# Kernel optimization log

Measured on AMD Instinct MI355X. Metric: run time of the kernel, lower is better.

The kernel has to match this reference:

```python
import jax, jax.numpy as jnp
import numpy as np

N_ENSEMBLE = 50
STATE_DIM = 32
ACTION_DIM = 8
HIDDEN = 256
BATCH = 8192
OUT_DIM = STATE_DIM + 1  # next_state + reward


def setup_inputs() -> dict:
    key = jax.random.key(0)
    ks = jax.random.split(key, 8)
    s = 0.05  # small init scale to keep activations sane
    return {
        "state": jax.random.normal(ks[0], (BATCH, STATE_DIM), dtype=jnp.float32),
        "action": jax.random.normal(ks[1], (BATCH, ACTION_DIM), dtype=jnp.float32),
        "W1": jax.random.normal(ks[2], (N_ENSEMBLE, STATE_DIM + ACTION_DIM, HIDDEN), dtype=jnp.float32) * s,
        "b1": jnp.zeros((N_ENSEMBLE, HIDDEN), dtype=jnp.float32),
        "W2": jax.random.normal(ks[3], (N_ENSEMBLE, HIDDEN, HIDDEN), dtype=jnp.float32) * s,
        "b2": jnp.zeros((N_ENSEMBLE, HIDDEN), dtype=jnp.float32),
        "W3": jax.random.normal(ks[4], (N_ENSEMBLE, HIDDEN, HIDDEN), dtype=jnp.float32) * s,
        "b3": jnp.zeros((N_ENSEMBLE, HIDDEN), dtype=jnp.float32),
        "W4": jax.random.normal(ks[5], (N_ENSEMBLE, HIDDEN, OUT_DIM), dtype=jnp.float32) * s,
        "b4": jnp.zeros((N_ENSEMBLE, OUT_DIM), dtype=jnp.float32),
    }


def reference(state, action, W1, b1, W2, b2, W3, b3, W4, b4):
    # state_action: [B, S+A] shared across all ensemble members
    sa = jnp.concatenate((state, action), axis=1)
    # Batched-over-ensemble GEMMs replace the python loop over 50 MLPs.
    # h: [B, E, H]
    h = jax.nn.relu(jnp.einsum("bi,eih->beh", sa, W1) + b1)
    h = jax.nn.relu(jnp.einsum("beh,ehk->bek", h, W2) + b2)
    h = jax.nn.relu(jnp.einsum("beh,ehk->bek", h, W3) + b3)
    preds = jnp.einsum("beh,eho->beo", h, W4) + b4  # [B, E, S+1]
    return preds[..., :-1], preds[..., -1]
```

## Files before the change

kernel.cpp:

```cpp
#include <hip/hip_runtime.h>


typedef __attribute__((ext_vector_type(8))) short short8;
typedef __attribute__((ext_vector_type(4))) float floatx4;

#define NE 50
#define NB 8192
#define OUT_NS_ELEMS (NB * NE * 32)
#define OSTRIDE 48

__device__ __forceinline__ unsigned short f2bf_rne(float x) {
  unsigned u = __float_as_uint(x);
  u += 0x7fffu + ((u >> 16) & 1u);
  return (unsigned short)(u >> 16);
}
__device__ __forceinline__ float bf2f(unsigned short b) {
  return __uint_as_float(((unsigned)b) << 16);
}
__device__ __forceinline__ floatx4 mfma16(short8 a, short8 b, floatx4 c) {
  return __builtin_amdgcn_mfma_f32_16x16x32_bf16(a, b, c, 0, 0, 0);
}
__device__ __forceinline__ unsigned pack_bf2(float lo, float hi) {
  unsigned u0 = __float_as_uint(lo) + 0x8000u;
  unsigned u1 = __float_as_uint(hi) + 0x8000u;
  return __builtin_amdgcn_perm(u1, u0, 0x07060302u);
}

__device__ __forceinline__ unsigned short load_bf(const void* p, long i, bool isbf) {
  if (isbf) return ((const unsigned short*)p)[i];
  return f2bf_rne(((const float*)p)[i]);
}
__device__ __forceinline__ float load_f(const void* p, long i, bool isbf) {
  if (isbf) return bf2f(((const unsigned short*)p)[i]);
  return ((const float*)p)[i];
}

__device__ void pack_w_panel(const void* __restrict__ src, unsigned short* __restrict__ dst,
                             bool isbf, int e, int kt, int K, int N, int NT, int perE,
                             unsigned short* lds) {
  const int t = threadIdx.x;
  const int Npad = NT * 16;
  const int NP = Npad + 10;
  if (!isbf && N == Npad) {
    const int nq = Npad >> 2;
    for (int idx = t; idx < 32 * nq; idx += 256) {
      int r = idx / nq, q = idx - r * nq;
      int k = kt * 32 + r;
      unsigned short v0 = 0, v1 = 0, v2 = 0, v3 = 0;
      if (k < K) {
        const float4 f =
            *(const float4*)((const float*)src + ((long)(e * K + k) * N + q * 4));
        v0 = f2bf_rne(f.x); v1 = f2bf_rne(f.y);
        v2 = f2bf_rne(f.z); v3 = f2bf_rne(f.w);
      }
      unsigned* p = (unsigned*)(lds + r * NP + q * 4);
      p[0] = (unsigned)v0 | ((unsigned)v1 << 16);
      p[1] = (unsigned)v2 | ((unsigned)v3 << 16);
    }
  } else if (isbf && N == Npad) {
    const int no = Npad >> 3;
    for (int idx = t; idx < 32 * no; idx += 256) {
      int r = idx / no, q = idx - r * no;
      int k = kt * 32 + r;
      uint4 f = make_uint4(0u, 0u, 0u, 0u);
      if (k < K)
        f = *(const uint4*)((const unsigned short*)src + ((long)(e * K + k) * N + q * 8));
      unsigned* p = (unsigned*)(lds + r * NP + q * 8);
      p[0] = f.x; p[1] = f.y; p[2] = f.z; p[3] = f.w;
    }
  } else {
    for (int idx = t; idx < 32 * Npad; idx += 256) {
      int r = idx / Npad, c = idx - r * Npad;
      int k = kt * 32 + r;
      unsigned short v = 0;
      if (k < K && c < N) v = load_bf(src, (long)(e * K + k) * N + c, isbf);
      lds[r * NP + c] = v;
    }
  }
  __syncthreads();
  for (int u = t; u < NT * 64; u += 256) {
    int nt = u >> 6, kb = (u >> 4) & 3, ni = u & 15;
    int n = nt * 16 + ni;
    unsigned v[4];
#pragma unroll
    for (int p = 0; p < 4; ++p) {
      unsigned lo = lds[(kb * 8 + 2 * p) * NP + n];
      unsigned hi = lds[(kb * 8 + 2 * p + 1) * NP + n];
      v[p] = lo | (hi << 16);
    }
    long off = (long)e * perE + ((long)((kt * NT + nt) * 64 + kb * 16 + ni)) * 8;
    *(uint4*)(dst + off) = make_uint4(v[0], v[1], v[2], v[3]);
  }
}

__global__ void k_pack(const void* __restrict__ state, const void* __restrict__ action,
                       const void* __restrict__ W1, const void* __restrict__ W2,
                       const void* __restrict__ W3, const void* __restrict__ W4,
                       const void* __restrict__ b1, const void* __restrict__ b2,
                       const void* __restrict__ b3, const void* __restrict__ b4,
                       int isbfi,
                       unsigned short* __restrict__ saP, unsigned short* __restrict__ w1P,
                       unsigned short* __restrict__ w2P, unsigned short* __restrict__ w3P,
                       unsigned short* __restrict__ w4P, float* __restrict__ biasP) {
  __shared__ unsigned short lds[32 * 266];
  const bool isbf = (isbfi != 0);
  const int b = blockIdx.x;
  if (b < 400) {
    pack_w_panel(W2, w2P, isbf, b >> 3, b & 7, 256, 256, 16, 65536, lds);
  } else if (b < 800) {
    int bb = b - 400;
    pack_w_panel(W3, w3P, isbf, bb >> 3, bb & 7, 256, 256, 16, 65536, lds);
  } else if (b < 900) {
    int bb = b - 800;
    pack_w_panel(W1, w1P, isbf, bb >> 1, bb & 1, 40, 256, 16, 16384, lds);
  } else if (b < 1300) {
    int bb = b - 900;
    pack_w_panel(W4, w4P, isbf, bb >> 3, bb & 7, 256, 33, 3, 12288, lds);
  } else if (b < 1556) {
    int u = (b - 1300) * 256 + threadIdx.x;
    int mi = u & 15, kb = (u >> 4) & 7, mt = u >> 7;
    int row = mt * 16 + mi;
    unsigned v[4] = {0u, 0u, 0u, 0u};
    if (kb < 4) {
#pragma unroll
      for (int p = 0; p < 4; ++p) {
        unsigned lo = load_bf(state, (long)row * 32 + kb * 8 + 2 * p, isbf);
        unsigned hi = load_bf(state, (long)row * 32 + kb * 8 + 2 * p + 1, isbf);
        v[p] = lo | (hi << 16);
      }
    } else if (kb == 4) {
#pragma unroll
      for (int p = 0; p < 4; ++p) {
        unsigned lo = load_bf(action, (long)row * 8 + 2 * p, isbf);
        unsigned hi = load_bf(action, (long)row * 8 + 2 * p + 1, isbf);
        v[p] = lo | (hi << 16);
      }
    }
    *(uint4*)(saP + (long)u * 8) = make_uint4(v[0], v[1], v[2], v[3]);
  } else {
    int gid = (b - 1556) * 256 + threadIdx.x;
    if (gid < NE * 816) {
      int e = gid / 816, r = gid - e * 816;
      float v = 0.0f;
      if (r < 256)      v = load_f(b1, e * 256 + r,         isbf);
      else if (r < 512) v = load_f(b2, e * 256 + (r - 256), isbf);
      else if (r < 768) v = load_f(b3, e * 256 + (r - 512), isbf);
      else { int q = r - 768; if (q < 33) v = load_f(b4, e * 33 + q, isbf); }
      biasP[gid] = v;
    }
  }
}


__device__ __forceinline__ void store_tile16(const floatx4& a4, unsigned short* hT,
                                             int FT, int BT, int li, int g) {
  int k0 = FT * 16 + g * 4;
  unsigned d0 = pack_bf2(fmaxf(a4[0], 0.0f), fmaxf(a4[1], 0.0f));
  unsigned d1 = pack_bf2(fmaxf(a4[2], 0.0f), fmaxf(a4[3], 0.0f));
  int addr = ((k0 >> 5) * 4 + BT) * 512 + ((k0 >> 3) & 3) * 128 + li * 8 + (k0 & 7);
  *(unsigned long long*)(hT + addr) =
      (unsigned long long)d0 | ((unsigned long long)d1 << 32);
}

__device__ __forceinline__ void hidden_layer(const unsigned short* __restrict__ wp,
                                             const float* __restrict__ br,
                                             unsigned short* hT,
                                             int wf, int l, int li, int g) {
  floatx4 acc[4][4];
#pragma unroll
  for (int ot = 0; ot < 4; ++ot) {
    const float4 bq = *(const float4*)(br + wf * 64 + ot * 16 + g * 4);
    floatx4 iv = {bq.x, bq.y, bq.z, bq.w};
#pragma unroll
    for (int bt = 0; bt < 4; ++bt) acc[ot][bt] = iv;
  }
#pragma unroll
  for (int kt = 0; kt < 8; ++kt) {
    short8 a[4];
#pragma unroll
    for (int ot = 0; ot < 4; ++ot)
      a[ot] = *(const short8*)(wp + (long)((kt * 16 + wf * 4 + ot) * 64 + l) * 8);
#pragma unroll
    for (int bt = 0; bt < 4; ++bt) {
      short8 b = *(const short8*)(hT + ((kt * 4 + bt) * 64 + l) * 8);
#pragma unroll
      for (int ot = 0; ot < 4; ++ot)
        acc[ot][bt] = mfma16(a[ot], b, acc[ot][bt]);
    }
  }
  __syncthreads();
#pragma unroll
  for (int ot = 0; ot < 4; ++ot)
#pragma unroll
    for (int bt = 0; bt < 4; ++bt)
      store_tile16(acc[ot][bt], hT, wf * 4 + ot, bt, li, g);
  __syncthreads();
}

__global__ __launch_bounds__(256, 4) void k_mlp(
    const unsigned short* __restrict__ sa,
    const unsigned short* __restrict__ w1,
    const unsigned short* __restrict__ w2,
    const unsigned short* __restrict__ w3,
    const unsigned short* __restrict__ w4,
    const float* __restrict__ bias,
    int isbfi,
    float* __restrict__ rewardWS,
    void* __restrict__ outp) {
  __shared__ __attribute__((aligned(16))) unsigned short hT[16384];
  const int tid = threadIdx.x;
  const int wf = tid >> 6, l = tid & 63, li = l & 15, g = l >> 4;

  const int lid = blockIdx.y * 128 + blockIdx.x;
  const int swz = (lid & 7) * 800 + (lid >> 3);
  const int e  = swz >> 7;
  const int bb = swz & 127;

  const float* brow = bias + e * 816;
  const bool isbf = (isbfi != 0);

  {
    floatx4 acc[4][4];
#pragma unroll
    for (int ot = 0; ot < 4; ++ot) {
      const float4 bq = *(const float4*)(brow + wf * 64 + ot * 16 + g * 4);
      floatx4 iv = {bq.x, bq.y, bq.z, bq.w};
#pragma unroll
      for (int bt = 0; bt < 4; ++bt) acc[ot][bt] = iv;
    }
#pragma unroll
    for (int kt = 0; kt < 2; ++kt) {
      short8 a[4];
#pragma unroll
      for (int ot = 0; ot < 4; ++ot)
        a[ot] = *(const short8*)(w1 + (long)e * 16384 +
                                 (long)((kt * 16 + wf * 4 + ot) * 64 + l) * 8);
#pragma unroll
      for (int bt = 0; bt < 4; ++bt) {
        short8 b = *(const short8*)(sa + (long)((bb * 4 + bt) * 128 + kt * 64 + l) * 8);
#pragma unroll
        for (int ot = 0; ot < 4; ++ot)
          acc[ot][bt] = mfma16(a[ot], b, acc[ot][bt]);
      }
    }
#pragma unroll
    for (int ot = 0; ot < 4; ++ot)
#pragma unroll
      for (int bt = 0; bt < 4; ++bt)
        store_tile16(acc[ot][bt], hT, wf * 4 + ot, bt, li, g);
    __syncthreads();
  }

  hidden_layer(w2 + (long)e * 65536, brow + 256, hT, wf, l, li, g);
  hidden_layer(w3 + (long)e * 65536, brow + 512, hT, wf, l, li, g);

  const float* brow4 = brow + 768;
  floatx4 acc4[3];
#pragma unroll
  for (int ft = 0; ft < 3; ++ft) {
    const float4 bq = *(const float4*)(brow4 + ft * 16 + g * 4);
    floatx4 iv = {bq.x, bq.y, bq.z, bq.w};
    acc4[ft] = iv;
  }
#pragma unroll
  for (int kt = 0; kt < 8; ++kt) {
    short8 a[3];
#pragma unroll
    for (int ft = 0; ft < 3; ++ft)
      a[ft] = *(const short8*)(w4 + (long)e * 12288 + (long)((kt * 3 + ft) * 64 + l) * 8);
    short8 b = *(const short8*)(hT + ((kt * 4 + wf) * 64 + l) * 8);
#pragma unroll
    for (int ft = 0; ft < 3; ++ft)
      acc4[ft] = mfma16(a[ft], b, acc4[ft]);
  }

  if (g == 0) {
    rewardWS[(long)e * NB + bb * 64 + wf * 16 + li] = acc4[2][0];
  }

  __syncthreads();
#pragma unroll
  for (int ft = 0; ft < 2; ++ft) {
    int batch = wf * 16 + li;
    unsigned d0 = pack_bf2(acc4[ft][0], acc4[ft][1]);
    unsigned d1 = pack_bf2(acc4[ft][2], acc4[ft][3]);
    *(unsigned long long*)(hT + batch * OSTRIDE + ft * 16 + g * 4) =
        (unsigned long long)d0 | ((unsigned long long)d1 << 32);
  }
  __syncthreads();

  if (isbf) {
    unsigned short* o16 = (unsigned short*)outp;
    int batch = tid >> 2;
    int chunk = tid & 3;
    uint4 v = *(const uint4*)(hT + batch * OSTRIDE + chunk * 8);
    *(uint4*)(o16 + ((long)(bb * 64 + batch) * NE + e) * 32 + chunk * 8) = v;
  } else {
    float* o32 = (float*)outp;
#pragma unroll
    for (int p = 0; p < 2; ++p) {
      int idx = p * 256 + tid;
      int batch = idx >> 3;
      int chunk = idx & 7;
      const unsigned short* s = hT + batch * OSTRIDE + chunk * 4;
      *(float4*)(o32 + ((long)(bb * 64 + batch) * NE + e) * 32 + chunk * 4) =
          make_float4(bf2f(s[0]), bf2f(s[1]), bf2f(s[2]), bf2f(s[3]));
    }
  }
}

__global__ void k_reward(const float* __restrict__ rw, int isbfi,
                         void* __restrict__ outp) {
  int id = blockIdx.x * 256 + threadIdx.x;
  if (id >= NB * NE) return;
  int b = id / NE, e = id - b * NE;
  float v = rw[(long)e * NB + b];
  if (isbfi != 0) {
    unsigned u = __float_as_uint(v) + 0x8000u;
    ((unsigned short*)outp)[OUT_NS_ELEMS + id] = (unsigned short)(u >> 16);
  } else {
    ((float*)outp)[OUT_NS_ELEMS + id] = v;
  }
}

extern "C" void kernel_launch(void* const* d_in, const int* in_sizes, int n_in,
                              void* d_out, int out_size, void* d_ws, size_t ws_size,
                              hipStream_t stream) {
  const void* state  = d_in[0];
  const void* action = d_in[1];
  const void* W1 = d_in[2];
  const void* b1 = d_in[3];
  const void* W2 = d_in[4];
  const void* b2 = d_in[5];
  const void* W3 = d_in[6];
  const void* b3 = d_in[7];
  const void* W4 = d_in[8];
  const void* b4 = d_in[9];
  (void)n_in; (void)out_size; (void)ws_size;

  const int isbf = (in_sizes[4] == NE * 256 * 256 * 2) ? 1 : 0;

  char* ws = (char*)d_ws;
  unsigned short* saP    = (unsigned short*)(ws + 256);
  unsigned short* w1P    = (unsigned short*)(ws + 1048832);
  unsigned short* w2P    = (unsigned short*)(ws + 2687232);
  unsigned short* w3P    = (unsigned short*)(ws + 9240832);
  unsigned short* w4P    = (unsigned short*)(ws + 15794432);
  float* biasP           = (float*)(ws + 17023232);
  float* rewardWS        = (float*)(ws + 17186432);

  k_pack<<<1716, 256, 0, stream>>>(state, action, W1, W2, W3, W4, b1, b2, b3, b4,
                                   isbf, saP, w1P, w2P, w3P, w4P, biasP);
  k_mlp<<<dim3(128, 50), 256, 0, stream>>>(saP, w1P, w2P, w3P, w4P, biasP, isbf,
                                           rewardWS, d_out);
  k_reward<<<(NB * NE + 255) / 256, 256, 0, stream>>>(rewardWS, isbf, d_out);
}
```

Baseline: 236.3 us.

## Halve per-block batch tile to 32 rows to double grid and raise occupancy

Each block of the fused MLP kernel now handles 32 batch rows instead of 64. This halves the accumulator registers and the LDS hidden buffer, doubles the grid to 256x50 blocks, and raises the launch-bounds occupancy hint from 4 to 5. The final layer's work is redistributed across the four waves: two compute next-state tiles and two compute reward. The aim is more resident waves for latency hiding, paid for with twice as many weight reloads per batch row and more blocks overall.

```diff
diff --git a/kernel.cpp b/kernel.cpp
--- a/kernel.cpp
+++ b/kernel.cpp
@@ -157,7 +157,7 @@
   int k0 = FT * 16 + g * 4;
   unsigned d0 = pack_bf2(fmaxf(a4[0], 0.0f), fmaxf(a4[1], 0.0f));
   unsigned d1 = pack_bf2(fmaxf(a4[2], 0.0f), fmaxf(a4[3], 0.0f));
-  int addr = ((k0 >> 5) * 4 + BT) * 512 + ((k0 >> 3) & 3) * 128 + li * 8 + (k0 & 7);
+  int addr = ((k0 >> 5) * 2 + BT) * 512 + ((k0 >> 3) & 3) * 128 + li * 8 + (k0 & 7);
   *(unsigned long long*)(hT + addr) =
       (unsigned long long)d0 | ((unsigned long long)d1 << 32);
 }
@@ -166,13 +166,13 @@
                                              const float* __restrict__ br,
                                              unsigned short* hT,
                                              int wf, int l, int li, int g) {
-  floatx4 acc[4][4];
+  floatx4 acc[4][2];
 #pragma unroll
   for (int ot = 0; ot < 4; ++ot) {
     const float4 bq = *(const float4*)(br + wf * 64 + ot * 16 + g * 4);
     floatx4 iv = {bq.x, bq.y, bq.z, bq.w};
 #pragma unroll
-    for (int bt = 0; bt < 4; ++bt) acc[ot][bt] = iv;
+    for (int bt = 0; bt < 2; ++bt) acc[ot][bt] = iv;
   }
 #pragma unroll
   for (int kt = 0; kt < 8; ++kt) {
@@ -181,8 +181,8 @@
     for (int ot = 0; ot < 4; ++ot)
       a[ot] = *(const short8*)(wp + (long)((kt * 16 + wf * 4 + ot) * 64 + l) * 8);
 #pragma unroll
-    for (int bt = 0; bt < 4; ++bt) {
-      short8 b = *(const short8*)(hT + ((kt * 4 + bt) * 64 + l) * 8);
+    for (int bt = 0; bt < 2; ++bt) {
+      short8 b = *(const short8*)(hT + ((kt * 2 + bt) * 64 + l) * 8);
 #pragma unroll
       for (int ot = 0; ot < 4; ++ot)
         acc[ot][bt] = mfma16(a[ot], b, acc[ot][bt]);
@@ -192,12 +192,12 @@
 #pragma unroll
   for (int ot = 0; ot < 4; ++ot)
 #pragma unroll
-    for (int bt = 0; bt < 4; ++bt)
+    for (int bt = 0; bt < 2; ++bt)
       store_tile16(acc[ot][bt], hT, wf * 4 + ot, bt, li, g);
   __syncthreads();
 }
 
-__global__ __launch_bounds__(256, 4) void k_mlp(
+__global__ __launch_bounds__(256, 5) void k_mlp(
     const unsigned short* __restrict__ sa,
     const unsigned short* __restrict__ w1,
     const unsigned short* __restrict__ w2,
@@ -207,26 +207,26 @@
     int isbfi,
     float* __restrict__ rewardWS,
     void* __restrict__ outp) {
-  __shared__ __attribute__((aligned(16))) unsigned short hT[16384];
+  __shared__ __attribute__((aligned(16))) unsigned short hT[8192];
   const int tid = threadIdx.x;
   const int wf = tid >> 6, l = tid & 63, li = l & 15, g = l >> 4;
 
-  const int lid = blockIdx.y * 128 + blockIdx.x;
-  const int swz = (lid & 7) * 800 + (lid >> 3);
-  const int e  = swz >> 7;
-  const int bb = swz & 127;
+  const int lid = blockIdx.y * 256 + blockIdx.x;
+  const int swz = (lid & 7) * 1600 + (lid >> 3);
+  const int e  = swz >> 8;
+  const int bb = swz & 255;
 
   const float* brow = bias + e * 816;
   const bool isbf = (isbfi != 0);
 
   {
-    floatx4 acc[4][4];
+    floatx4 acc[4][2];
 #pragma unroll
     for (int ot = 0; ot < 4; ++ot) {
       const float4 bq = *(const float4*)(brow + wf * 64 + ot * 16 + g * 4);
       floatx4 iv = {bq.x, bq.y, bq.z, bq.w};
 #pragma unroll
-      for (int bt = 0; bt < 4; ++bt) acc[ot][bt] = iv;
+      for (int bt = 0; bt < 2; ++bt) acc[ot][bt] = iv;
     }
 #pragma unroll
     for (int kt = 0; kt < 2; ++kt) {
@@ -236,8 +236,8 @@
         a[ot] = *(const short8*)(w1 + (long)e * 16384 +
                                  (long)((kt * 16 + wf * 4 + ot) * 64 + l) * 8);
 #pragma unroll
-      for (int bt = 0; bt < 4; ++bt) {
-        short8 b = *(const short8*)(sa + (long)((bb * 4 + bt) * 128 + kt * 64 + l) * 8);
+      for (int bt = 0; bt < 2; ++bt) {
+        short8 b = *(const short8*)(sa + (long)((bb * 2 + bt) * 128 + kt * 64 + l) * 8);
 #pragma unroll
         for (int ot = 0; ot < 4; ++ot)
           acc[ot][bt] = mfma16(a[ot], b, acc[ot][bt]);
@@ -246,7 +246,7 @@
 #pragma unroll
     for (int ot = 0; ot < 4; ++ot)
 #pragma unroll
-      for (int bt = 0; bt < 4; ++bt)
+      for (int bt = 0; bt < 2; ++bt)
         store_tile16(acc[ot][bt], hT, wf * 4 + ot, bt, li, g);
     __syncthreads();
   }
@@ -255,57 +255,63 @@
   hidden_layer(w3 + (long)e * 65536, brow + 512, hT, wf, l, li, g);
 
   const float* brow4 = brow + 768;
-  floatx4 acc4[3];
-#pragma unroll
-  for (int ft = 0; ft < 3; ++ft) {
-    const float4 bq = *(const float4*)(brow4 + ft * 16 + g * 4);
-    floatx4 iv = {bq.x, bq.y, bq.z, bq.w};
-    acc4[ft] = iv;
+  const int bl = wf & 1;
+  const int nft = (wf < 2) ? 2 : 1;
+  const int f0 = (wf < 2) ? 0 : 2;
+  floatx4 acc4[2];
+#pragma unroll
+  for (int ft = 0; ft < 2; ++ft) {
+    if (ft < nft) {
+      const float4 bq = *(const float4*)(brow4 + (f0 + ft) * 16 + g * 4);
+      floatx4 iv = {bq.x, bq.y, bq.z, bq.w};
+      acc4[ft] = iv;
+    }
   }
 #pragma unroll
   for (int kt = 0; kt < 8; ++kt) {
-    short8 a[3];
-#pragma unroll
-    for (int ft = 0; ft < 3; ++ft)
-      a[ft] = *(const short8*)(w4 + (long)e * 12288 + (long)((kt * 3 + ft) * 64 + l) * 8);
-    short8 b = *(const short8*)(hT + ((kt * 4 + wf) * 64 + l) * 8);
-#pragma unroll
-    for (int ft = 0; ft < 3; ++ft)
-      acc4[ft] = mfma16(a[ft], b, acc4[ft]);
-  }
-
-  if (g == 0) {
-    rewardWS[(long)e * NB + bb * 64 + wf * 16 + li] = acc4[2][0];
-  }
-
-  __syncthreads();
-#pragma unroll
-  for (int ft = 0; ft < 2; ++ft) {
-    int batch = wf * 16 + li;
-    unsigned d0 = pack_bf2(acc4[ft][0], acc4[ft][1]);
-    unsigned d1 = pack_bf2(acc4[ft][2], acc4[ft][3]);
-    *(unsigned long long*)(hT + batch * OSTRIDE + ft * 16 + g * 4) =
-        (unsigned long long)d0 | ((unsigned long long)d1 << 32);
+    short8 b = *(const short8*)(hT + ((kt * 2 + bl) * 64 + l) * 8);
+#pragma unroll
+    for (int ft = 0; ft < 2; ++ft) {
+      if (ft < nft) {
+        short8 a = *(const short8*)(w4 + (long)e * 12288 +
+                                    (long)((kt * 3 + f0 + ft) * 64 + l) * 8);
+        acc4[ft] = mfma16(a, b, acc4[ft]);
+      }
+    }
+  }
+
+  if (wf >= 2 && g == 0) {
+    rewardWS[(long)e * NB + bb * 32 + bl * 16 + li] = acc4[0][0];
+  }
+
+  __syncthreads();
+  if (wf < 2) {
+#pragma unroll
+    for (int ft = 0; ft < 2; ++ft) {
+      int batch = bl * 16 + li;
+      unsigned d0 = pack_bf2(acc4[ft][0], acc4[ft][1]);
+      unsigned d1 = pack_bf2(acc4[ft][2], acc4[ft][3]);
+      *(unsigned long long*)(hT + batch * OSTRIDE + ft * 16 + g * 4) =
+          (unsigned long long)d0 | ((unsigned long long)d1 << 32);
+    }
   }
   __syncthreads();
 
   if (isbf) {
-    unsigned short* o16 = (unsigned short*)outp;
-    int batch = tid >> 2;
-    int chunk = tid & 3;
-    uint4 v = *(const uint4*)(hT + batch * OSTRIDE + chunk * 8);
-    *(uint4*)(o16 + ((long)(bb * 64 + batch) * NE + e) * 32 + chunk * 8) = v;
+    if (tid < 128) {
+      unsigned short* o16 = (unsigned short*)outp;
+      int batch = tid >> 2;
+      int chunk = tid & 3;
+      uint4 v = *(const uint4*)(hT + batch * OSTRIDE + chunk * 8);
+      *(uint4*)(o16 + ((long)(bb * 32 + batch) * NE + e) * 32 + chunk * 8) = v;
+    }
   } else {
     float* o32 = (float*)outp;
-#pragma unroll
-    for (int p = 0; p < 2; ++p) {
-      int idx = p * 256 + tid;
-      int batch = idx >> 3;
-      int chunk = idx & 7;
-      const unsigned short* s = hT + batch * OSTRIDE + chunk * 4;
-      *(float4*)(o32 + ((long)(bb * 64 + batch) * NE + e) * 32 + chunk * 4) =
-          make_float4(bf2f(s[0]), bf2f(s[1]), bf2f(s[2]), bf2f(s[3]));
-    }
+    int batch = tid >> 3;
+    int chunk = tid & 7;
+    const unsigned short* s = hT + batch * OSTRIDE + chunk * 4;
+    *(float4*)(o32 + ((long)(bb * 32 + batch) * NE + e) * 32 + chunk * 4) =
+        make_float4(bf2f(s[0]), bf2f(s[1]), bf2f(s[2]), bf2f(s[3]));
   }
 }
 
@@ -351,7 +357,7 @@
 
   k_pack<<<1716, 256, 0, stream>>>(state, action, W1, W2, W3, W4, b1, b2, b3, b4,
                                    isbf, saP, w1P, w2P, w3P, w4P, biasP);
-  k_mlp<<<dim3(128, 50), 256, 0, stream>>>(saP, w1P, w2P, w3P, w4P, biasP, isbf,
+  k_mlp<<<dim3(256, 50), 256, 0, stream>>>(saP, w1P, w2P, w3P, w4P, biasP, isbf,
                                            rewardWS, d_out);
   k_reward<<<(NB * NE + 255) / 256, 256, 0, stream>>>(rewardWS, isbf, d_out);
 }
```

Result: slower. 276.6 us (+17.1%).

## Switch hidden layers from 16x16x32 to 32x32x16 bf16 MFMA tiles

Applied to the files above, without the earlier changes.

Replaces the 16x16x32 MFMA tiling of layers 1-3 with 32x32x16 MFMA. Each wave now computes a 2x2 grid of 32x32 output tiles instead of a 4x4 grid of 16x16 tiles. The weight and input packing, the activation LDS layout and the store routine are rewritten to match the 32x32 operand fragment layout, and the layer-4 B-operand read is re-indexed accordingly. The aim is fewer MFMA issues and fewer LDS and global operand loads per FLOP. The risk is different LDS bank-conflict patterns and longer MFMA dependency latency.

```diff
diff --git a/kernel.cpp b/kernel.cpp
--- a/kernel.cpp
+++ b/kernel.cpp
@@ -3,6 +3,7 @@
 
 typedef __attribute__((ext_vector_type(8))) short short8;
 typedef __attribute__((ext_vector_type(4))) float floatx4;
+typedef __attribute__((ext_vector_type(16))) float floatx16;
 
 #define NE 50
 #define NB 8192
@@ -20,6 +21,9 @@
 __device__ __forceinline__ floatx4 mfma16(short8 a, short8 b, floatx4 c) {
   return __builtin_amdgcn_mfma_f32_16x16x32_bf16(a, b, c, 0, 0, 0);
 }
+__device__ __forceinline__ floatx16 mfma32(short8 a, short8 b, floatx16 c) {
+  return __builtin_amdgcn_mfma_f32_32x32x16_bf16(a, b, c, 0, 0, 0);
+}
 __device__ __forceinline__ unsigned pack_bf2(float lo, float hi) {
   unsigned u0 = __float_as_uint(lo) + 0x8000u;
   unsigned u1 = __float_as_uint(hi) + 0x8000u;
@@ -36,8 +40,8 @@
 }
 
 __device__ void pack_w_panel(const void* __restrict__ src, unsigned short* __restrict__ dst,
-                             bool isbf, int e, int kt, int K, int N, int NT, int perE,
-                             unsigned short* lds) {
+                             bool isbf, bool fmt32, int e, int kt, int K, int N, int NT,
+                             int perE, unsigned short* lds) {
   const int t = threadIdx.x;
   const int Npad = NT * 16;
   const int NP = Npad + 10;
@@ -78,18 +82,40 @@
     }
   }
   __syncthreads();
-  for (int u = t; u < NT * 64; u += 256) {
-    int nt = u >> 6, kb = (u >> 4) & 3, ni = u & 15;
-    int n = nt * 16 + ni;
-    unsigned v[4];
-#pragma unroll
-    for (int p = 0; p < 4; ++p) {
-      unsigned lo = lds[(kb * 8 + 2 * p) * NP + n];
-      unsigned hi = lds[(kb * 8 + 2 * p + 1) * NP + n];
-      v[p] = lo | (hi << 16);
-    }
-    long off = (long)e * perE + ((long)((kt * NT + nt) * 64 + kb * 16 + ni)) * 8;
-    *(uint4*)(dst + off) = make_uint4(v[0], v[1], v[2], v[3]);
+  if (fmt32) {
+    const int NMT = NT >> 1;
+    const int per_ku = NMT * 64;
+    for (int u = t; u < NT * 64; u += 256) {
+      int ku_loc = u / per_ku;
+      int rem = u - ku_loc * per_ku;
+      int mu = rem >> 6, lane = rem & 63;
+      int m = mu * 32 + (lane & 31);
+      int rowbase = ku_loc * 16 + (lane >> 5) * 8;
+      unsigned v[4];
+#pragma unroll
+      for (int p = 0; p < 4; ++p) {
+        unsigned lo = lds[(rowbase + 2 * p) * NP + m];
+        unsigned hi = lds[(rowbase + 2 * p + 1) * NP + m];
+        v[p] = lo | (hi << 16);
+      }
+      long off = (long)e * perE +
+                 ((long)(((kt * 2 + ku_loc) * NMT + mu) * 64 + lane)) * 8;
+      *(uint4*)(dst + off) = make_uint4(v[0], v[1], v[2], v[3]);
+    }
+  } else {
+    for (int u = t; u < NT * 64; u += 256) {
+      int nt = u >> 6, kb = (u >> 4) & 3, ni = u & 15;
+      int n = nt * 16 + ni;
+      unsigned v[4];
+#pragma unroll
+      for (int p = 0; p < 4; ++p) {
+        unsigned lo = lds[(kb * 8 + 2 * p) * NP + n];
+        unsigned hi = lds[(kb * 8 + 2 * p + 1) * NP + n];
+        v[p] = lo | (hi << 16);
+      }
+      long off = (long)e * perE + ((long)((kt * NT + nt) * 64 + kb * 16 + ni)) * 8;
+      *(uint4*)(dst + off) = make_uint4(v[0], v[1], v[2], v[3]);
+    }
   }
 }
 
@@ -106,33 +132,34 @@
   const bool isbf = (isbfi != 0);
   const int b = blockIdx.x;
   if (b < 400) {
-    pack_w_panel(W2, w2P, isbf, b >> 3, b & 7, 256, 256, 16, 65536, lds);
+    pack_w_panel(W2, w2P, isbf, true, b >> 3, b & 7, 256, 256, 16, 65536, lds);
   } else if (b < 800) {
     int bb = b - 400;
-    pack_w_panel(W3, w3P, isbf, bb >> 3, bb & 7, 256, 256, 16, 65536, lds);
+    pack_w_panel(W3, w3P, isbf, true, bb >> 3, bb & 7, 256, 256, 16, 65536, lds);
   } else if (b < 900) {
     int bb = b - 800;
-    pack_w_panel(W1, w1P, isbf, bb >> 1, bb & 1, 40, 256, 16, 16384, lds);
+    pack_w_panel(W1, w1P, isbf, true, bb >> 1, bb & 1, 40, 256, 16, 16384, lds);
   } else if (b < 1300) {
     int bb = b - 900;
-    pack_w_panel(W4, w4P, isbf, bb >> 3, bb & 7, 256, 33, 3, 12288, lds);
+    pack_w_panel(W4, w4P, isbf, false, bb >> 3, bb & 7, 256, 33, 3, 12288, lds);
   } else if (b < 1556) {
     int u = (b - 1300) * 256 + threadIdx.x;
-    int mi = u & 15, kb = (u >> 4) & 7, mt = u >> 7;
-    int row = mt * 16 + mi;
+    int lane = u & 63, ku = (u >> 6) & 3, bt32 = u >> 8;
+    int n = bt32 * 32 + (lane & 31);
+    int kb = ku * 16 + (lane >> 5) * 8;
     unsigned v[4] = {0u, 0u, 0u, 0u};
-    if (kb < 4) {
+    if (kb < 32) {
 #pragma unroll
       for (int p = 0; p < 4; ++p) {
-        unsigned lo = load_bf(state, (long)row * 32 + kb * 8 + 2 * p, isbf);
-        unsigned hi = load_bf(state, (long)row * 32 + kb * 8 + 2 * p + 1, isbf);
+        unsigned lo = load_bf(state, (long)n * 32 + kb + 2 * p, isbf);
+        unsigned hi = load_bf(state, (long)n * 32 + kb + 2 * p + 1, isbf);
         v[p] = lo | (hi << 16);
       }
-    } else if (kb == 4) {
+    } else if (kb == 32) {
 #pragma unroll
       for (int p = 0; p < 4; ++p) {
-        unsigned lo = load_bf(action, (long)row * 8 + 2 * p, isbf);
-        unsigned hi = load_bf(action, (long)row * 8 + 2 * p + 1, isbf);
+        unsigned lo = load_bf(action, (long)n * 8 + 2 * p, isbf);
+        unsigned hi = load_bf(action, (long)n * 8 + 2 * p + 1, isbf);
         v[p] = lo | (hi << 16);
       }
     }
@@ -152,48 +179,54 @@
 }
 
 
-__device__ __forceinline__ void store_tile16(const floatx4& a4, unsigned short* hT,
-                                             int FT, int BT, int li, int g) {
-  int k0 = FT * 16 + g * 4;
-  unsigned d0 = pack_bf2(fmaxf(a4[0], 0.0f), fmaxf(a4[1], 0.0f));
-  unsigned d1 = pack_bf2(fmaxf(a4[2], 0.0f), fmaxf(a4[3], 0.0f));
-  int addr = ((k0 >> 5) * 4 + BT) * 512 + ((k0 >> 3) & 3) * 128 + li * 8 + (k0 & 7);
-  *(unsigned long long*)(hT + addr) =
-      (unsigned long long)d0 | ((unsigned long long)d1 << 32);
+__device__ __forceinline__ void store_tile32(const floatx16& A, unsigned short* hT,
+                                             int FT32, int BT, int col, int hi) {
+  unsigned d[8];
+#pragma unroll
+  for (int q = 0; q < 8; ++q)
+    d[q] = pack_bf2(fmaxf(A[2 * q], 0.0f), fmaxf(A[2 * q + 1], 0.0f));
+#pragma unroll
+  for (int w = 0; w < 4; ++w) {
+    int addr = (((FT32 * 2 + (w >> 1)) * 2 + BT) * 64 + col + 32 * (w & 1)) * 8 + 4 * hi;
+    *(unsigned long long*)(hT + addr) =
+        (unsigned long long)d[2 * w] | ((unsigned long long)d[2 * w + 1] << 32);
+  }
 }
 
 __device__ __forceinline__ void hidden_layer(const unsigned short* __restrict__ wp,
                                              const float* __restrict__ br,
                                              unsigned short* hT,
-                                             int wf, int l, int li, int g) {
-  floatx4 acc[4][4];
-#pragma unroll
-  for (int ot = 0; ot < 4; ++ot) {
-    const float4 bq = *(const float4*)(br + wf * 64 + ot * 16 + g * 4);
-    floatx4 iv = {bq.x, bq.y, bq.z, bq.w};
-#pragma unroll
-    for (int bt = 0; bt < 4; ++bt) acc[ot][bt] = iv;
-  }
-#pragma unroll
-  for (int kt = 0; kt < 8; ++kt) {
-    short8 a[4];
-#pragma unroll
-    for (int ot = 0; ot < 4; ++ot)
-      a[ot] = *(const short8*)(wp + (long)((kt * 16 + wf * 4 + ot) * 64 + l) * 8);
-#pragma unroll
-    for (int bt = 0; bt < 4; ++bt) {
-      short8 b = *(const short8*)(hT + ((kt * 4 + bt) * 64 + l) * 8);
-#pragma unroll
-      for (int ot = 0; ot < 4; ++ot)
-        acc[ot][bt] = mfma16(a[ot], b, acc[ot][bt]);
-    }
-  }
-  __syncthreads();
-#pragma unroll
-  for (int ot = 0; ot < 4; ++ot)
-#pragma unroll
-    for (int bt = 0; bt < 4; ++bt)
-      store_tile16(acc[ot][bt], hT, wf * 4 + ot, bt, li, g);
+                                             int wf, int l, int col, int hi) {
+  floatx16 acc[2][2];
+#pragma unroll
+  for (int ft = 0; ft < 2; ++ft) {
+    const float* bp = br + wf * 64 + ft * 32 + 4 * hi;
+    const float4 q0 = *(const float4*)(bp);
+    const float4 q1 = *(const float4*)(bp + 8);
+    const float4 q2 = *(const float4*)(bp + 16);
+    const float4 q3 = *(const float4*)(bp + 24);
+    floatx16 iv = {q0.x, q0.y, q0.z, q0.w, q1.x, q1.y, q1.z, q1.w,
+                   q2.x, q2.y, q2.z, q2.w, q3.x, q3.y, q3.z, q3.w};
+    acc[ft][0] = iv;
+    acc[ft][1] = iv;
+  }
+#pragma unroll
+  for (int ks = 0; ks < 16; ++ks) {
+    short8 a0 = *(const short8*)(wp + (long)((ks * 8 + 2 * wf + 0) * 64 + l) * 8);
+    short8 a1 = *(const short8*)(wp + (long)((ks * 8 + 2 * wf + 1) * 64 + l) * 8);
+#pragma unroll
+    for (int bt = 0; bt < 2; ++bt) {
+      short8 b = *(const short8*)(hT + ((ks * 2 + bt) * 64 + l) * 8);
+      acc[0][bt] = mfma32(a0, b, acc[0][bt]);
+      acc[1][bt] = mfma32(a1, b, acc[1][bt]);
+    }
+  }
+  __syncthreads();
+#pragma unroll
+  for (int ft = 0; ft < 2; ++ft)
+#pragma unroll
+    for (int bt = 0; bt < 2; ++bt)
+      store_tile32(acc[ft][bt], hT, wf * 2 + ft, bt, col, hi);
   __syncthreads();
 }
 
@@ -210,6 +243,7 @@
   __shared__ __attribute__((aligned(16))) unsigned short hT[16384];
   const int tid = threadIdx.x;
   const int wf = tid >> 6, l = tid & 63, li = l & 15, g = l >> 4;
+  const int col = l & 31, hi = l >> 5;
 
   const int lid = blockIdx.y * 128 + blockIdx.x;
   const int swz = (lid & 7) * 800 + (lid >> 3);
@@ -220,39 +254,42 @@
   const bool isbf = (isbfi != 0);
 
   {
-    floatx4 acc[4][4];
-#pragma unroll
-    for (int ot = 0; ot < 4; ++ot) {
-      const float4 bq = *(const float4*)(brow + wf * 64 + ot * 16 + g * 4);
-      floatx4 iv = {bq.x, bq.y, bq.z, bq.w};
-#pragma unroll
-      for (int bt = 0; bt < 4; ++bt) acc[ot][bt] = iv;
-    }
-#pragma unroll
-    for (int kt = 0; kt < 2; ++kt) {
-      short8 a[4];
-#pragma unroll
-      for (int ot = 0; ot < 4; ++ot)
-        a[ot] = *(const short8*)(w1 + (long)e * 16384 +
-                                 (long)((kt * 16 + wf * 4 + ot) * 64 + l) * 8);
-#pragma unroll
-      for (int bt = 0; bt < 4; ++bt) {
-        short8 b = *(const short8*)(sa + (long)((bb * 4 + bt) * 128 + kt * 64 + l) * 8);
-#pragma unroll
-        for (int ot = 0; ot < 4; ++ot)
-          acc[ot][bt] = mfma16(a[ot], b, acc[ot][bt]);
-      }
-    }
-#pragma unroll
-    for (int ot = 0; ot < 4; ++ot)
-#pragma unroll
-      for (int bt = 0; bt < 4; ++bt)
-        store_tile16(acc[ot][bt], hT, wf * 4 + ot, bt, li, g);
+    floatx16 acc[2][2];
+#pragma unroll
+    for (int ft = 0; ft < 2; ++ft) {
+      const float* bp = brow + wf * 64 + ft * 32 + 4 * hi;
+      const float4 q0 = *(const float4*)(bp);
+      const float4 q1 = *(const float4*)(bp + 8);
+      const float4 q2 = *(const float4*)(bp + 16);
+      const float4 q3 = *(const float4*)(bp + 24);
+      floatx16 iv = {q0.x, q0.y, q0.z, q0.w, q1.x, q1.y, q1.z, q1.w,
+                     q2.x, q2.y, q2.z, q2.w, q3.x, q3.y, q3.z, q3.w};
+      acc[ft][0] = iv;
+      acc[ft][1] = iv;
+    }
+#pragma unroll
+    for (int ks = 0; ks < 4; ++ks) {
+      short8 a0 = *(const short8*)(w1 + (long)e * 16384 +
+                                   (long)((ks * 8 + 2 * wf + 0) * 64 + l) * 8);
+      short8 a1 = *(const short8*)(w1 + (long)e * 16384 +
+                                   (long)((ks * 8 + 2 * wf + 1) * 64 + l) * 8);
+#pragma unroll
+      for (int bt = 0; bt < 2; ++bt) {
+        short8 b = *(const short8*)(sa + (long)(((bb * 2 + bt) * 4 + ks) * 64 + l) * 8);
+        acc[0][bt] = mfma32(a0, b, acc[0][bt]);
+        acc[1][bt] = mfma32(a1, b, acc[1][bt]);
+      }
+    }
+#pragma unroll
+    for (int ft = 0; ft < 2; ++ft)
+#pragma unroll
+      for (int bt = 0; bt < 2; ++bt)
+        store_tile32(acc[ft][bt], hT, wf * 2 + ft, bt, col, hi);
     __syncthreads();
   }
 
-  hidden_layer(w2 + (long)e * 65536, brow + 256, hT, wf, l, li, g);
-  hidden_layer(w3 + (long)e * 65536, brow + 512, hT, wf, l, li, g);
+  hidden_layer(w2 + (long)e * 65536, brow + 256, hT, wf, l, col, hi);
+  hidden_layer(w3 + (long)e * 65536, brow + 512, hT, wf, l, col, hi);
 
   const float* brow4 = brow + 768;
   floatx4 acc4[3];
@@ -268,7 +305,8 @@
 #pragma unroll
     for (int ft = 0; ft < 3; ++ft)
       a[ft] = *(const short8*)(w4 + (long)e * 12288 + (long)((kt * 3 + ft) * 64 + l) * 8);
-    short8 b = *(const short8*)(hT + ((kt * 4 + wf) * 64 + l) * 8);
+    short8 b = *(const short8*)(hT + (((kt * 2 + (l >> 5)) * 2 + (wf >> 1)) * 64 +
+                                      (wf & 1) * 16 + (l & 15) + 32 * ((l >> 4) & 1)) * 8);
 #pragma unroll
     for (int ft = 0; ft < 3; ++ft)
       acc4[ft] = mfma16(a[ft], b, acc4[ft]);
```

Result: slower. 250.5 us (+6.0%).
